# Kernel tuning notes

Hardware: AMD Instinct MI355X
Metric: run time of the kernel (lower is better)

Reference implementation:

```python
import jax, jax.numpy as jnp
import numpy as np

B, N, E = 2, 50000, 800000
IN, HID, OUT = 128, 64, 1
EPS = 1e-5


def setup_inputs() -> dict:
    key = jax.random.key(0)
    ks = jax.random.split(key, 13)
    x = jax.random.normal(ks[0], (B, N, IN), jnp.float32)
    edge_index = jax.random.randint(ks[1], (2, E), 0, N, dtype=jnp.int64)
    edge_weight = 0.1 * jax.random.normal(ks[2], (E,), jnp.float32)  # nn.Parameter, pre-exp
    W1 = jax.random.normal(ks[3], (IN, HID), jnp.float32) / np.sqrt(IN)
    b1 = jnp.zeros((HID,), jnp.float32)
    W2 = jax.random.normal(ks[4], (HID, HID), jnp.float32) / np.sqrt(HID)
    b2 = jnp.zeros((HID,), jnp.float32)
    g1 = jnp.ones((HID,), jnp.float32)
    be1 = jnp.zeros((HID,), jnp.float32)
    g2 = jnp.ones((HID,), jnp.float32)
    be2 = jnp.zeros((HID,), jnp.float32)
    Wc = jax.random.normal(ks[5], (HID, OUT), jnp.float32) / np.sqrt(HID)
    bc = jnp.zeros((OUT,), jnp.float32)
    return {"x": x, "edge_weight": edge_weight, "W1": W1, "b1": b1,
            "W2": W2, "b2": b2, "g1": g1, "be1": be1, "g2": g2, "be2": be2,
            "Wc": Wc, "bc": bc, "edge_index": edge_index}


def reference(x, edge_weight, W1, b1, W2, b2, g1, be1, g2, be2, Wc, bc, edge_index):
    n = x.shape[1]
    row, col = edge_index[0], edge_index[1]
    ew = jnp.exp(edge_weight)
    # GCN normalization with self-loops (fill_value=1), as in PyG gcn_norm
    loop = jnp.arange(n)
    rows = jnp.concatenate([row, loop])
    cols = jnp.concatenate([col, loop])
    w = jnp.concatenate([ew, jnp.ones((n,), ew.dtype)])
    deg = jax.ops.segment_sum(w, cols, num_segments=n)
    dinv = 1.0 / jnp.sqrt(deg)  # deg >= 1 due to self-loops
    norm = dinv[rows] * w * dinv[cols]  # [E+N]

    def conv(h, W, b):
        h = h @ W                                  # [B, N, H]
        msg = h[:, rows, :] * norm[None, :, None]  # gather + weight  [B, E+N, H]
        agg = jnp.zeros_like(h).at[:, cols, :].add(msg)  # scatter-add
        return agg + b

    def bn(h, g, be):  # BatchNorm1d over flattened (B*N, H), training-mode stats
        h2 = h.reshape(-1, h.shape[-1])
        m = h2.mean(axis=0)
        v = h2.var(axis=0)
        return (((h2 - m) / jnp.sqrt(v + EPS)) * g + be).reshape(h.shape)

    h = jax.nn.relu(conv(x, W1, b1))
    h = bn(h, g1, be1)  # dropout is identity in eval
    h = jax.nn.relu(conv(h, W2, b2))
    h = bn(h, g2, be2)
    out = (h @ Wc + bc)[..., 0]  # squeeze(-1) -> [B, N]
    return out
```

## Files before the change

kernel.cpp:

```cpp
#include <hip/hip_runtime.h>
#include <hip/hip_fp16.h>
#include <cstdint>
#include <cstddef>


#define CAP  64
#define OCAP 65536
#define BN_EPS 1e-5f

static __device__ __forceinline__ unsigned h2u(__half2 h) {
  union { __half2 h; unsigned u; } c; c.h = h; return c.u;
}
static __device__ __forceinline__ __half2 u2h(unsigned u) {
  union { unsigned u; __half2 h; } c; c.u = u; return c.h;
}
static __device__ __forceinline__ unsigned pack_pair(int src, float w) {
  __half hw = __float2half_rn(w);
  union { __half h; unsigned short s; } c; c.h = hw;
  return ((unsigned)src << 16) | c.s;
}
static __device__ __forceinline__ float pair_w(unsigned p) {
  union { unsigned short s; __half h; } c; c.s = (unsigned short)(p & 0xFFFFu);
  return __half2float(c.h);
}

__global__ void k_mega(const float* __restrict__ x, const float* __restrict__ W,
                       __half* __restrict__ out, int nrows, int N,
                       const float* __restrict__ ew, const int* __restrict__ ei,
                       int* __restrict__ cnt, unsigned* __restrict__ pairs,
                       int* __restrict__ ofl_cnt, int* __restrict__ ofl_list,
                       int E, int gemmBlocks, int fillBlocks) {
  constexpr int RT = 64, KC = 64, S = KC + 4;
  __shared__ float ws[KC * 64];
  __shared__ float xs[RT * S];

  int bid = blockIdx.x;
  int tid = threadIdx.x;
  int role = bid % 3;

  if (role == 0) {
    int gid = bid / 3;
    if (gid >= gemmBlocks) return;
    int row0 = gid * RT;
    int rg = tid >> 4, cg = tid & 15;
    int c0 = cg * 4, r0 = rg * 4;
    float acc[4][4];
#pragma unroll
    for (int i = 0; i < 4; ++i)
#pragma unroll
      for (int j = 0; j < 4; ++j) acc[i][j] = 0.0f;

    for (int ch = 0; ch < 2; ++ch) {
      if (ch) __syncthreads();
      const float4* Wp = (const float4*)(W + (size_t)ch * KC * 64);
      for (int s = tid; s < KC * 16; s += 256)
        ((float4*)ws)[s] = Wp[s];
      for (int s = tid; s < RT * 16; s += 256) {
        int r = s >> 4, k4 = s & 15;
        int gr = row0 + r;
        float4 v = make_float4(0.f, 0.f, 0.f, 0.f);
        if (gr < nrows)
          v = *(const float4*)(x + (size_t)gr * 128 + ch * KC + k4 * 4);
        *(float4*)&xs[r * S + k4 * 4] = v;
      }
      __syncthreads();
#pragma unroll 2
      for (int kk = 0; kk < KC; kk += 4) {
        float4 wv0 = *(const float4*)&ws[(kk + 0) * 64 + c0];
        float4 wv1 = *(const float4*)&ws[(kk + 1) * 64 + c0];
        float4 wv2 = *(const float4*)&ws[(kk + 2) * 64 + c0];
        float4 wv3 = *(const float4*)&ws[(kk + 3) * 64 + c0];
#pragma unroll
        for (int i = 0; i < 4; ++i) {
          float4 xv = *(const float4*)&xs[(r0 + i) * S + kk];
          acc[i][0] = fmaf(xv.x, wv0.x, acc[i][0]);
          acc[i][1] = fmaf(xv.x, wv0.y, acc[i][1]);
          acc[i][2] = fmaf(xv.x, wv0.z, acc[i][2]);
          acc[i][3] = fmaf(xv.x, wv0.w, acc[i][3]);
          acc[i][0] = fmaf(xv.y, wv1.x, acc[i][0]);
          acc[i][1] = fmaf(xv.y, wv1.y, acc[i][1]);
          acc[i][2] = fmaf(xv.y, wv1.z, acc[i][2]);
          acc[i][3] = fmaf(xv.y, wv1.w, acc[i][3]);
          acc[i][0] = fmaf(xv.z, wv2.x, acc[i][0]);
          acc[i][1] = fmaf(xv.z, wv2.y, acc[i][1]);
          acc[i][2] = fmaf(xv.z, wv2.z, acc[i][2]);
          acc[i][3] = fmaf(xv.z, wv2.w, acc[i][3]);
          acc[i][0] = fmaf(xv.w, wv3.x, acc[i][0]);
          acc[i][1] = fmaf(xv.w, wv3.y, acc[i][1]);
          acc[i][2] = fmaf(xv.w, wv3.z, acc[i][2]);
          acc[i][3] = fmaf(xv.w, wv3.w, acc[i][3]);
        }
      }
    }
#pragma unroll
    for (int i = 0; i < 4; ++i) {
      int gr = row0 + r0 + i;
      if (gr < nrows) {
        int orow = (gr < N) ? gr * 2 : (gr - N) * 2 + 1;
        __half2 h01 = __floats2half2_rn(acc[i][0], acc[i][1]);
        __half2 h23 = __floats2half2_rn(acc[i][2], acc[i][3]);
        *(uint2*)(out + (size_t)orow * 64 + c0) = make_uint2(h2u(h01), h2u(h23));
      }
    }
  } else {
    int fid = (bid / 3) * 2 + role - 1;
    if (fid >= fillBlocks) return;
    int e = fid * 256 + tid;
    if (e >= E) return;
    int r = ei[e];
    int c = ei[(size_t)E + e];
    float w = expf(ew[e]);
    int pos = atomicAdd(&cnt[c], 1);
    if (pos < CAP) {
      pairs[(size_t)c * CAP + pos] = pack_pair(r, w);
    } else {
      int o = atomicAdd(ofl_cnt, 1);
      if (o < OCAP) ofl_list[o] = e;
    }
  }
}

__global__ void k_degb(const unsigned* __restrict__ pairs, const int* __restrict__ cnt,
                       float* __restrict__ deg, int N) {
  int node = blockIdx.x * 4 + (threadIdx.x >> 6);
  if (node >= N) return;
  int lane = threadIdx.x & 63;
  int n = cnt[node];
  n = n > CAP ? CAP : n;
  float v = 0.0f;
  if (lane < n) v = pair_w(pairs[(size_t)node * CAP + lane]);
#pragma unroll
  for (int off = 32; off > 0; off >>= 1) v += __shfl_xor(v, off, 64);
  if (lane == 0) deg[node] = v + 1.0f;
}

__global__ void k_dego(const float* __restrict__ ew, const int* __restrict__ ei,
                       const int* __restrict__ ofl_cnt, const int* __restrict__ ofl_list,
                       float* __restrict__ deg, int E) {
  int tot = *ofl_cnt;
  if (tot > OCAP) tot = OCAP;
  for (int i = blockIdx.x * blockDim.x + threadIdx.x; i < tot;
       i += gridDim.x * blockDim.x) {
    int e = ofl_list[i];
    atomicAdd(&deg[ei[(size_t)E + e]], expf(ew[e]));
  }
}

__global__ void k_dinvf(float* __restrict__ deg, int N) {
  int i = blockIdx.x * blockDim.x + threadIdx.x;
  if (i < N) deg[i] = rsqrtf(deg[i]);
}

__global__ void k_gemm2(const __half* __restrict__ in, const float* __restrict__ W,
                        __half* __restrict__ out, int nrows,
                        const float* __restrict__ bias, const float* __restrict__ scsh) {
  constexpr int RT = 64, KC = 64, S = KC + 4;
  __shared__ float ws[KC * 64];
  __shared__ float xs[RT * S];

  int tid = threadIdx.x;
  int row0 = blockIdx.x * RT;
  for (int s = tid; s < KC * 16; s += 256)
    ((float4*)ws)[s] = ((const float4*)W)[s];
  for (int s = tid; s < RT * 16; s += 256) {
    int r = s >> 4, k4 = s & 15;
    int gr = row0 + r;
    int kg = k4 * 4;
    float4 v = make_float4(0.f, 0.f, 0.f, 0.f);
    if (gr < nrows) {
      uint2 u = *(const uint2*)(in + (size_t)gr * 64 + kg);
      float2 fa = __half22float2(u2h(u.x));
      float2 fb = __half22float2(u2h(u.y));
      v = make_float4(fa.x, fa.y, fb.x, fb.y);
    }
    float4 bb = *(const float4*)(bias + kg);
    float4 sc = *(const float4*)(scsh + kg);
    float4 sh = *(const float4*)(scsh + 64 + kg);
    v.x = fmaxf(v.x + bb.x, 0.f) * sc.x + sh.x;
    v.y = fmaxf(v.y + bb.y, 0.f) * sc.y + sh.y;
    v.z = fmaxf(v.z + bb.z, 0.f) * sc.z + sh.z;
    v.w = fmaxf(v.w + bb.w, 0.f) * sc.w + sh.w;
    *(float4*)&xs[r * S + kg] = v;
  }
  __syncthreads();

  int rg = tid >> 4, cg = tid & 15;
  int c0 = cg * 4, r0 = rg * 4;
  float acc[4][4];
#pragma unroll
  for (int i = 0; i < 4; ++i)
#pragma unroll
    for (int j = 0; j < 4; ++j) acc[i][j] = 0.0f;
#pragma unroll 2
  for (int kk = 0; kk < KC; kk += 4) {
    float4 wv0 = *(const float4*)&ws[(kk + 0) * 64 + c0];
    float4 wv1 = *(const float4*)&ws[(kk + 1) * 64 + c0];
    float4 wv2 = *(const float4*)&ws[(kk + 2) * 64 + c0];
    float4 wv3 = *(const float4*)&ws[(kk + 3) * 64 + c0];
#pragma unroll
    for (int i = 0; i < 4; ++i) {
      float4 xv = *(const float4*)&xs[(r0 + i) * S + kk];
      acc[i][0] = fmaf(xv.x, wv0.x, acc[i][0]);
      acc[i][1] = fmaf(xv.x, wv0.y, acc[i][1]);
      acc[i][2] = fmaf(xv.x, wv0.z, acc[i][2]);
      acc[i][3] = fmaf(xv.x, wv0.w, acc[i][3]);
      acc[i][0] = fmaf(xv.y, wv1.x, acc[i][0]);
      acc[i][1] = fmaf(xv.y, wv1.y, acc[i][1]);
      acc[i][2] = fmaf(xv.y, wv1.z, acc[i][2]);
      acc[i][3] = fmaf(xv.y, wv1.w, acc[i][3]);
      acc[i][0] = fmaf(xv.z, wv2.x, acc[i][0]);
      acc[i][1] = fmaf(xv.z, wv2.y, acc[i][1]);
      acc[i][2] = fmaf(xv.z, wv2.z, acc[i][2]);
      acc[i][3] = fmaf(xv.z, wv2.w, acc[i][3]);
      acc[i][0] = fmaf(xv.w, wv3.x, acc[i][0]);
      acc[i][1] = fmaf(xv.w, wv3.y, acc[i][1]);
      acc[i][2] = fmaf(xv.w, wv3.z, acc[i][2]);
      acc[i][3] = fmaf(xv.w, wv3.w, acc[i][3]);
    }
  }
#pragma unroll
  for (int i = 0; i < 4; ++i) {
    int gr = row0 + r0 + i;
    if (gr < nrows) {
      __half2 h01 = __floats2half2_rn(acc[i][0], acc[i][1]);
      __half2 h23 = __floats2half2_rn(acc[i][2], acc[i][3]);
      *(uint2*)(out + (size_t)gr * 64 + c0) = make_uint2(h2u(h01), h2u(h23));
    }
  }
}

__global__ void k_agg(const __half* __restrict__ h, const unsigned* __restrict__ pairs,
                      const int* __restrict__ cnt, const float* __restrict__ dinv,
                      __half* __restrict__ raw, int N) {
  int node = blockIdx.x * 4 + (threadIdx.x >> 6);
  if (node >= N) return;
  int lane = threadIdx.x & 63;
  const __half2* hv = (const __half2*)h;
  float dc = dinv[node];
  float2 self = __half22float2(hv[(size_t)node * 64 + lane]);
  float2 acc = make_float2(self.x * dc, self.y * dc);
  int n = cnt[node];
  n = n > CAP ? CAP : n;
  const unsigned* pp = pairs + (size_t)node * CAP;
  int k = 0;
  for (; k + 12 <= n; k += 12) {
    unsigned p[12];
#pragma unroll
    for (int q = 0; q < 12; ++q) p[q] = pp[k + q];
    float dr[12];
#pragma unroll
    for (int q = 0; q < 12; ++q) dr[q] = dinv[p[q] >> 16];
    __half2 v[12];
#pragma unroll
    for (int q = 0; q < 12; ++q) v[q] = hv[(size_t)(p[q] >> 16) * 64 + lane];
#pragma unroll
    for (int q = 0; q < 12; ++q) {
      float w = pair_w(p[q]) * dr[q];
      float2 f = __half22float2(v[q]);
      acc.x = fmaf(w, f.x, acc.x);
      acc.y = fmaf(w, f.y, acc.y);
    }
  }
  for (; k + 4 <= n; k += 4) {
    unsigned p[4];
#pragma unroll
    for (int q = 0; q < 4; ++q) p[q] = pp[k + q];
    float dr[4];
#pragma unroll
    for (int q = 0; q < 4; ++q) dr[q] = dinv[p[q] >> 16];
    __half2 v[4];
#pragma unroll
    for (int q = 0; q < 4; ++q) v[q] = hv[(size_t)(p[q] >> 16) * 64 + lane];
#pragma unroll
    for (int q = 0; q < 4; ++q) {
      float w = pair_w(p[q]) * dr[q];
      float2 f = __half22float2(v[q]);
      acc.x = fmaf(w, f.x, acc.x);
      acc.y = fmaf(w, f.y, acc.y);
    }
  }
  for (; k < n; ++k) {
    unsigned p = pp[k];
    float w = pair_w(p) * dinv[p >> 16];
    float2 f = __half22float2(hv[(size_t)(p >> 16) * 64 + lane]);
    acc.x = fmaf(w, f.x, acc.x);
    acc.y = fmaf(w, f.y, acc.y);
  }
  ((__half2*)raw)[(size_t)node * 64 + lane] =
      __floats2half2_rn(acc.x * dc, acc.y * dc);
}

__global__ void k_ofl(const float* __restrict__ ew, const int* __restrict__ ei,
                      const float* __restrict__ dinv, const int* __restrict__ ofl_cnt,
                      const int* __restrict__ ofl_list,
                      const __half* __restrict__ h, __half* __restrict__ raw,
                      int N, int E) {
  int tot = *ofl_cnt;
  if (tot > OCAP) tot = OCAP;
  for (int i = blockIdx.x * blockDim.x + threadIdx.x; i < tot;
       i += gridDim.x * blockDim.x) {
    int e = ofl_list[i];
    int r = ei[e];
    int c = ei[(size_t)E + e];
    float nrm = dinv[r] * expf(ew[e]) * dinv[c];
    const __half2* hr = (const __half2*)(h + (size_t)r * 128);
    unsigned* dst = (unsigned*)(raw + (size_t)c * 128);
    for (int j = 0; j < 64; ++j) {
      float2 hv2 = __half22float2(hr[j]);
      unsigned old = dst[j], assumed;
      do {
        assumed = old;
        float2 cur = __half22float2(u2h(assumed));
        __half2 nv = __floats2half2_rn(cur.x + nrm * hv2.x, cur.y + nrm * hv2.y);
        old = atomicCAS(&dst[j], assumed, h2u(nv));
      } while (old != assumed);
    }
  }
}

__global__ void k_stats(const __half* __restrict__ raw, const float* __restrict__ bias,
                        float* __restrict__ stats, const float* __restrict__ g,
                        const float* __restrict__ be, float* __restrict__ scsh,
                        int* __restrict__ done, float invCnt, int rows) {
  __shared__ float S[256], Q[256];
  __shared__ int isLast;
  int tid = threadIdx.x;
  int c = tid & 63, rg = tid >> 6;
  float s = 0.0f, q = 0.0f;
  for (int r = blockIdx.x * 4 + rg; r < rows; r += gridDim.x * 4) {
    float y = fmaxf(__half2float(raw[(size_t)r * 64 + c]) + bias[c], 0.0f);
    s += y;
    q += y * y;
  }
  S[tid] = s; Q[tid] = q;
  __syncthreads();
  if (tid < 64) {
    float ts = S[tid] + S[tid + 64] + S[tid + 128] + S[tid + 192];
    float tq = Q[tid] + Q[tid + 64] + Q[tid + 128] + Q[tid + 192];
    atomicAdd(&stats[tid], ts);
    atomicAdd(&stats[64 + tid], tq);
  }
  __threadfence();
  if (tid == 0) {
    int old = atomicAdd(done, 1);
    isLast = (old == (int)gridDim.x - 1);
  }
  __syncthreads();
  if (isLast && tid < 64) {
    __threadfence();
    float m = atomicAdd(&stats[tid], 0.0f) * invCnt;
    float qq = atomicAdd(&stats[64 + tid], 0.0f) * invCnt;
    float v = qq - m * m;
    v = v < 0.0f ? 0.0f : v;
    float inv = rsqrtf(v + BN_EPS);
    float sc = g[tid] * inv;
    scsh[tid] = sc;
    scsh[64 + tid] = be[tid] - m * sc;
  }
}

__global__ void k_out(const __half* __restrict__ raw, const float* __restrict__ bias,
                      const float* __restrict__ scsh, const float* __restrict__ Wc,
                      const float* __restrict__ bc, float* __restrict__ out,
                      int rows, int N) {
  int row = blockIdx.x * 4 + (threadIdx.x >> 6);
  int c = threadIdx.x & 63;
  if (row >= rows) return;
  float v = fmaxf(__half2float(raw[(size_t)row * 64 + c]) + bias[c], 0.0f)
              * scsh[c] + scsh[64 + c];
  float p = v * Wc[c];
#pragma unroll
  for (int off = 32; off > 0; off >>= 1) p += __shfl_xor(p, off, 64);
  if (c == 0) {
    int node = row >> 1, b = row & 1;
    out[(size_t)b * N + node] = p + bc[0];
  }
}

extern "C" void kernel_launch(void* const* d_in, const int* in_sizes, int n_in,
                              void* d_out, int out_size, void* d_ws, size_t ws_size,
                              hipStream_t stream) {
  const float* x   = (const float*)d_in[0];
  const float* ew  = (const float*)d_in[1];
  const float* W1  = (const float*)d_in[2];
  const float* b1  = (const float*)d_in[3];
  const float* W2  = (const float*)d_in[4];
  const float* b2  = (const float*)d_in[5];
  const float* g1  = (const float*)d_in[6];
  const float* be1 = (const float*)d_in[7];
  const float* g2  = (const float*)d_in[8];
  const float* be2 = (const float*)d_in[9];
  const float* Wc  = (const float*)d_in[10];
  const float* bc  = (const float*)d_in[11];
  const int*   ei  = (const int*)d_in[12];

  const int E  = in_sizes[1];
  const int BN = in_sizes[0] / 128;
  const int N  = BN / 2;

  char* w = (char*)d_ws;
  size_t off = 0;
  int*   cnt    = (int*)  (w + off); off += (size_t)N * 4;
  float* stats1 = (float*)(w + off); off += 512;
  float* stats2 = (float*)(w + off); off += 512;
  int*   oflc   = (int*)  (w + off); off += 16;
  int*   done1  = (int*)  (w + off); off += 16;
  int*   done2  = (int*)  (w + off); off += 16;
  size_t zbytes = off;
  float* dinv   = (float*)(w + off); off += (size_t)N * 4;
  float* scsh1  = (float*)(w + off); off += 512;
  float* scsh2  = (float*)(w + off); off += 512;
  int*   ofll   = (int*)  (w + off); off += (size_t)OCAP * 4;
  off = (off + 255) & ~(size_t)255;
  unsigned* pairs = (unsigned*)(w + off); off += (size_t)N * CAP * 4;
  __half* bufA  = (__half*)(w + off); off += (size_t)BN * 64 * 2;
  __half* bufB  = (__half*)(w + off); off += (size_t)BN * 64 * 2;

  float* out = (float*)d_out;

  hipMemsetAsync(w, 0, zbytes, stream);

  dim3 blk(256);
  int gB = (BN + 63) / 64;
  int fB = (E + 255) / 256;
  int base3 = gB > (fB + 1) / 2 ? gB : (fB + 1) / 2;
  int gMega = 3 * base3;
  int gN  = (N + 255) / 256;
  int gR  = (BN + 3) / 4;
  int gA  = (N + 3) / 4;

  k_mega<<<gMega, blk, 0, stream>>>(x, W1, bufA, BN, N, ew, ei, cnt, pairs,
                                    oflc, ofll, E, gB, fB);
  k_degb<<<gA, blk, 0, stream>>>(pairs, cnt, dinv, N);
  k_dego<<<16, blk, 0, stream>>>(ew, ei, oflc, ofll, dinv, E);
  k_dinvf<<<gN, blk, 0, stream>>>(dinv, N);

  k_agg<<<gA, blk, 0, stream>>>(bufA, pairs, cnt, dinv, bufB, N);
  k_ofl<<<16, blk, 0, stream>>>(ew, ei, dinv, oflc, ofll, bufA, bufB, N, E);
  k_stats<<<400, blk, 0, stream>>>(bufB, b1, stats1, g1, be1, scsh1, done1,
                                   1.0f / (float)BN, BN);

  k_gemm2<<<gB, blk, 0, stream>>>(bufB, W2, bufA, BN, b1, scsh1);
  k_agg<<<gA, blk, 0, stream>>>(bufA, pairs, cnt, dinv, bufB, N);
  k_ofl<<<16, blk, 0, stream>>>(ew, ei, dinv, oflc, ofll, bufA, bufB, N, E);
  k_stats<<<400, blk, 0, stream>>>(bufB, b2, stats2, g2, be2, scsh2, done2,
                                   1.0f / (float)BN, BN);

  k_out<<<gR, blk, 0, stream>>>(bufB, b2, scsh2, Wc, bc, out, BN, N);
}
```

Measured before the change: 366.5 us.

## Fuse whole GCN pipeline into one persistent cooperative kernel with grid syncs

Replaces the chain of about a dozen kernel launches with a single cooperative persistent kernel that walks through edge bucketing, GEMM1, degree computation, aggregation, BN statistics, GEMM2 and the output projection, separated by grid-wide syncs. BN statistics are now folded into the aggregation pass as per-block partial sums, removing the separate stats kernels and their global atomics. When overflow edges exist, a recompute pass runs after the fixup. This removes launch gaps and redundant reads of the aggregated buffer, but fixes the grid size to occupancy times 256 blocks (capped at 1024), so each phase gets lower parallelism and pays grid-sync overhead.

```diff
diff --git a/kernel.cpp b/kernel.cpp
--- a/kernel.cpp
+++ b/kernel.cpp
@@ -1,12 +1,16 @@
 #include <hip/hip_runtime.h>
 #include <hip/hip_fp16.h>
+#include <hip/hip_cooperative_groups.h>
 #include <cstdint>
 #include <cstddef>
+
+namespace cg = cooperative_groups;
 
 
 #define CAP  64
 #define OCAP 65536
 #define BN_EPS 1e-5f
+#define MAXB 1024
 
 static __device__ __forceinline__ unsigned h2u(__half2 h) {
   union { __half2 h; unsigned u; } c; c.h = h; return c.u;
@@ -24,182 +28,116 @@
   return __half2float(c.h);
 }
 
-__global__ void k_mega(const float* __restrict__ x, const float* __restrict__ W,
-                       __half* __restrict__ out, int nrows, int N,
-                       const float* __restrict__ ew, const int* __restrict__ ei,
-                       int* __restrict__ cnt, unsigned* __restrict__ pairs,
-                       int* __restrict__ ofl_cnt, int* __restrict__ ofl_list,
-                       int E, int gemmBlocks, int fillBlocks) {
-  constexpr int RT = 64, KC = 64, S = KC + 4;
-  __shared__ float ws[KC * 64];
-  __shared__ float xs[RT * S];
-
-  int bid = blockIdx.x;
-  int tid = threadIdx.x;
-  int role = bid % 3;
-
-  if (role == 0) {
-    int gid = bid / 3;
-    if (gid >= gemmBlocks) return;
-    int row0 = gid * RT;
-    int rg = tid >> 4, cg = tid & 15;
-    int c0 = cg * 4, r0 = rg * 4;
-    float acc[4][4];
-#pragma unroll
-    for (int i = 0; i < 4; ++i)
-#pragma unroll
-      for (int j = 0; j < 4; ++j) acc[i][j] = 0.0f;
-
-    for (int ch = 0; ch < 2; ++ch) {
-      if (ch) __syncthreads();
-      const float4* Wp = (const float4*)(W + (size_t)ch * KC * 64);
-      for (int s = tid; s < KC * 16; s += 256)
-        ((float4*)ws)[s] = Wp[s];
-      for (int s = tid; s < RT * 16; s += 256) {
-        int r = s >> 4, k4 = s & 15;
-        int gr = row0 + r;
-        float4 v = make_float4(0.f, 0.f, 0.f, 0.f);
-        if (gr < nrows)
-          v = *(const float4*)(x + (size_t)gr * 128 + ch * KC + k4 * 4);
-        *(float4*)&xs[r * S + k4 * 4] = v;
+struct Params {
+  const float* x; const float* ew;
+  const float* W1; const float* b1; const float* W2; const float* b2;
+  const float* g1; const float* be1; const float* g2; const float* be2;
+  const float* Wc; const float* bc; const int* ei;
+  int* cnt; int* oflc; int* ofll;
+  unsigned* pairs; float* dinv; float* pst;
+  float* scsh1; float* scsh2;
+  __half* bufA; __half* bufB; float* out;
+  int E, N, BN, gB;
+};
+
+static __device__ void gemm1_tile(const Params& p, int row0, float* ws, float* xs) {
+  const int tid = threadIdx.x;
+  __syncthreads();
+  int rg = tid >> 4, cgi = tid & 15, c0 = cgi * 4, r0 = rg * 4;
+  float acc[4][4];
+#pragma unroll
+  for (int i = 0; i < 4; ++i)
+#pragma unroll
+    for (int j = 0; j < 4; ++j) acc[i][j] = 0.0f;
+  for (int ch = 0; ch < 2; ++ch) {
+    if (ch) __syncthreads();
+    const float4* Wp = (const float4*)(p.W1 + (size_t)ch * 64 * 64);
+    for (int s = tid; s < 64 * 16; s += 256) ((float4*)ws)[s] = Wp[s];
+    for (int s = tid; s < 64 * 16; s += 256) {
+      int r = s >> 4, k4 = s & 15, gr = row0 + r;
+      float4 v = make_float4(0.f, 0.f, 0.f, 0.f);
+      if (gr < p.BN) v = *(const float4*)(p.x + (size_t)gr * 128 + ch * 64 + k4 * 4);
+      *(float4*)&xs[r * 68 + k4 * 4] = v;
+    }
+    __syncthreads();
+#pragma unroll 2
+    for (int kk = 0; kk < 64; kk += 4) {
+      float4 wv0 = *(const float4*)&ws[(kk + 0) * 64 + c0];
+      float4 wv1 = *(const float4*)&ws[(kk + 1) * 64 + c0];
+      float4 wv2 = *(const float4*)&ws[(kk + 2) * 64 + c0];
+      float4 wv3 = *(const float4*)&ws[(kk + 3) * 64 + c0];
+#pragma unroll
+      for (int i = 0; i < 4; ++i) {
+        float4 xv = *(const float4*)&xs[(r0 + i) * 68 + kk];
+        acc[i][0] = fmaf(xv.x, wv0.x, acc[i][0]);
+        acc[i][1] = fmaf(xv.x, wv0.y, acc[i][1]);
+        acc[i][2] = fmaf(xv.x, wv0.z, acc[i][2]);
+        acc[i][3] = fmaf(xv.x, wv0.w, acc[i][3]);
+        acc[i][0] = fmaf(xv.y, wv1.x, acc[i][0]);
+        acc[i][1] = fmaf(xv.y, wv1.y, acc[i][1]);
+        acc[i][2] = fmaf(xv.y, wv1.z, acc[i][2]);
+        acc[i][3] = fmaf(xv.y, wv1.w, acc[i][3]);
+        acc[i][0] = fmaf(xv.z, wv2.x, acc[i][0]);
+        acc[i][1] = fmaf(xv.z, wv2.y, acc[i][1]);
+        acc[i][2] = fmaf(xv.z, wv2.z, acc[i][2]);
+        acc[i][3] = fmaf(xv.z, wv2.w, acc[i][3]);
+        acc[i][0] = fmaf(xv.w, wv3.x, acc[i][0]);
+        acc[i][1] = fmaf(xv.w, wv3.y, acc[i][1]);
+        acc[i][2] = fmaf(xv.w, wv3.z, acc[i][2]);
+        acc[i][3] = fmaf(xv.w, wv3.w, acc[i][3]);
       }
-      __syncthreads();
-#pragma unroll 2
-      for (int kk = 0; kk < KC; kk += 4) {
-        float4 wv0 = *(const float4*)&ws[(kk + 0) * 64 + c0];
-        float4 wv1 = *(const float4*)&ws[(kk + 1) * 64 + c0];
-        float4 wv2 = *(const float4*)&ws[(kk + 2) * 64 + c0];
-        float4 wv3 = *(const float4*)&ws[(kk + 3) * 64 + c0];
-#pragma unroll
-        for (int i = 0; i < 4; ++i) {
-          float4 xv = *(const float4*)&xs[(r0 + i) * S + kk];
-          acc[i][0] = fmaf(xv.x, wv0.x, acc[i][0]);
-          acc[i][1] = fmaf(xv.x, wv0.y, acc[i][1]);
-          acc[i][2] = fmaf(xv.x, wv0.z, acc[i][2]);
-          acc[i][3] = fmaf(xv.x, wv0.w, acc[i][3]);
-          acc[i][0] = fmaf(xv.y, wv1.x, acc[i][0]);
-          acc[i][1] = fmaf(xv.y, wv1.y, acc[i][1]);
-          acc[i][2] = fmaf(xv.y, wv1.z, acc[i][2]);
-          acc[i][3] = fmaf(xv.y, wv1.w, acc[i][3]);
-          acc[i][0] = fmaf(xv.z, wv2.x, acc[i][0]);
-          acc[i][1] = fmaf(xv.z, wv2.y, acc[i][1]);
-          acc[i][2] = fmaf(xv.z, wv2.z, acc[i][2]);
-          acc[i][3] = fmaf(xv.z, wv2.w, acc[i][3]);
-          acc[i][0] = fmaf(xv.w, wv3.x, acc[i][0]);
-          acc[i][1] = fmaf(xv.w, wv3.y, acc[i][1]);
-          acc[i][2] = fmaf(xv.w, wv3.z, acc[i][2]);
-          acc[i][3] = fmaf(xv.w, wv3.w, acc[i][3]);
-        }
-      }
-    }
-#pragma unroll
-    for (int i = 0; i < 4; ++i) {
-      int gr = row0 + r0 + i;
-      if (gr < nrows) {
-        int orow = (gr < N) ? gr * 2 : (gr - N) * 2 + 1;
-        __half2 h01 = __floats2half2_rn(acc[i][0], acc[i][1]);
-        __half2 h23 = __floats2half2_rn(acc[i][2], acc[i][3]);
-        *(uint2*)(out + (size_t)orow * 64 + c0) = make_uint2(h2u(h01), h2u(h23));
-      }
-    }
-  } else {
-    int fid = (bid / 3) * 2 + role - 1;
-    if (fid >= fillBlocks) return;
-    int e = fid * 256 + tid;
-    if (e >= E) return;
-    int r = ei[e];
-    int c = ei[(size_t)E + e];
-    float w = expf(ew[e]);
-    int pos = atomicAdd(&cnt[c], 1);
-    if (pos < CAP) {
-      pairs[(size_t)c * CAP + pos] = pack_pair(r, w);
-    } else {
-      int o = atomicAdd(ofl_cnt, 1);
-      if (o < OCAP) ofl_list[o] = e;
-    }
-  }
-}
-
-__global__ void k_degb(const unsigned* __restrict__ pairs, const int* __restrict__ cnt,
-                       float* __restrict__ deg, int N) {
-  int node = blockIdx.x * 4 + (threadIdx.x >> 6);
-  if (node >= N) return;
-  int lane = threadIdx.x & 63;
-  int n = cnt[node];
-  n = n > CAP ? CAP : n;
-  float v = 0.0f;
-  if (lane < n) v = pair_w(pairs[(size_t)node * CAP + lane]);
-#pragma unroll
-  for (int off = 32; off > 0; off >>= 1) v += __shfl_xor(v, off, 64);
-  if (lane == 0) deg[node] = v + 1.0f;
-}
-
-__global__ void k_dego(const float* __restrict__ ew, const int* __restrict__ ei,
-                       const int* __restrict__ ofl_cnt, const int* __restrict__ ofl_list,
-                       float* __restrict__ deg, int E) {
-  int tot = *ofl_cnt;
-  if (tot > OCAP) tot = OCAP;
-  for (int i = blockIdx.x * blockDim.x + threadIdx.x; i < tot;
-       i += gridDim.x * blockDim.x) {
-    int e = ofl_list[i];
-    atomicAdd(&deg[ei[(size_t)E + e]], expf(ew[e]));
-  }
-}
-
-__global__ void k_dinvf(float* __restrict__ deg, int N) {
-  int i = blockIdx.x * blockDim.x + threadIdx.x;
-  if (i < N) deg[i] = rsqrtf(deg[i]);
-}
-
-__global__ void k_gemm2(const __half* __restrict__ in, const float* __restrict__ W,
-                        __half* __restrict__ out, int nrows,
-                        const float* __restrict__ bias, const float* __restrict__ scsh) {
-  constexpr int RT = 64, KC = 64, S = KC + 4;
-  __shared__ float ws[KC * 64];
-  __shared__ float xs[RT * S];
-
-  int tid = threadIdx.x;
-  int row0 = blockIdx.x * RT;
-  for (int s = tid; s < KC * 16; s += 256)
-    ((float4*)ws)[s] = ((const float4*)W)[s];
-  for (int s = tid; s < RT * 16; s += 256) {
-    int r = s >> 4, k4 = s & 15;
-    int gr = row0 + r;
-    int kg = k4 * 4;
+    }
+  }
+#pragma unroll
+  for (int i = 0; i < 4; ++i) {
+    int gr = row0 + r0 + i;
+    if (gr < p.BN) {
+      int orow = (gr < p.N) ? gr * 2 : (gr - p.N) * 2 + 1;
+      __half2 h01 = __floats2half2_rn(acc[i][0], acc[i][1]);
+      __half2 h23 = __floats2half2_rn(acc[i][2], acc[i][3]);
+      *(uint2*)(p.bufA + (size_t)orow * 64 + c0) = make_uint2(h2u(h01), h2u(h23));
+    }
+  }
+}
+
+static __device__ void gemm2_tile(const Params& p, int row0, float* ws, float* xs) {
+  const int tid = threadIdx.x;
+  __syncthreads();
+  for (int s = tid; s < 64 * 16; s += 256) ((float4*)ws)[s] = ((const float4*)p.W2)[s];
+  for (int s = tid; s < 64 * 16; s += 256) {
+    int r = s >> 4, k4 = s & 15, gr = row0 + r, kg = k4 * 4;
     float4 v = make_float4(0.f, 0.f, 0.f, 0.f);
-    if (gr < nrows) {
-      uint2 u = *(const uint2*)(in + (size_t)gr * 64 + kg);
+    if (gr < p.BN) {
+      uint2 u = *(const uint2*)(p.bufB + (size_t)gr * 64 + kg);
       float2 fa = __half22float2(u2h(u.x));
       float2 fb = __half22float2(u2h(u.y));
       v = make_float4(fa.x, fa.y, fb.x, fb.y);
     }
-    float4 bb = *(const float4*)(bias + kg);
-    float4 sc = *(const float4*)(scsh + kg);
-    float4 sh = *(const float4*)(scsh + 64 + kg);
+    float4 bb = *(const float4*)(p.b1 + kg);
+    float4 sc = *(const float4*)(p.scsh1 + kg);
+    float4 sh = *(const float4*)(p.scsh1 + 64 + kg);
     v.x = fmaxf(v.x + bb.x, 0.f) * sc.x + sh.x;
     v.y = fmaxf(v.y + bb.y, 0.f) * sc.y + sh.y;
     v.z = fmaxf(v.z + bb.z, 0.f) * sc.z + sh.z;
     v.w = fmaxf(v.w + bb.w, 0.f) * sc.w + sh.w;
-    *(float4*)&xs[r * S + kg] = v;
-  }
-  __syncthreads();
-
-  int rg = tid >> 4, cg = tid & 15;
-  int c0 = cg * 4, r0 = rg * 4;
+    *(float4*)&xs[r * 68 + kg] = v;
+  }
+  __syncthreads();
+  int rg = tid >> 4, cgi = tid & 15, c0 = cgi * 4, r0 = rg * 4;
   float acc[4][4];
 #pragma unroll
   for (int i = 0; i < 4; ++i)
 #pragma unroll
     for (int j = 0; j < 4; ++j) acc[i][j] = 0.0f;
 #pragma unroll 2
-  for (int kk = 0; kk < KC; kk += 4) {
+  for (int kk = 0; kk < 64; kk += 4) {
     float4 wv0 = *(const float4*)&ws[(kk + 0) * 64 + c0];
     float4 wv1 = *(const float4*)&ws[(kk + 1) * 64 + c0];
     float4 wv2 = *(const float4*)&ws[(kk + 2) * 64 + c0];
     float4 wv3 = *(const float4*)&ws[(kk + 3) * 64 + c0];
 #pragma unroll
     for (int i = 0; i < 4; ++i) {
-      float4 xv = *(const float4*)&xs[(r0 + i) * S + kk];
+      float4 xv = *(const float4*)&xs[(r0 + i) * 68 + kk];
       acc[i][0] = fmaf(xv.x, wv0.x, acc[i][0]);
       acc[i][1] = fmaf(xv.x, wv0.y, acc[i][1]);
       acc[i][2] = fmaf(xv.x, wv0.z, acc[i][2]);
@@ -221,88 +159,120 @@
 #pragma unroll
   for (int i = 0; i < 4; ++i) {
     int gr = row0 + r0 + i;
-    if (gr < nrows) {
+    if (gr < p.BN) {
       __half2 h01 = __floats2half2_rn(acc[i][0], acc[i][1]);
       __half2 h23 = __floats2half2_rn(acc[i][2], acc[i][3]);
-      *(uint2*)(out + (size_t)gr * 64 + c0) = make_uint2(h2u(h01), h2u(h23));
-    }
-  }
-}
-
-__global__ void k_agg(const __half* __restrict__ h, const unsigned* __restrict__ pairs,
-                      const int* __restrict__ cnt, const float* __restrict__ dinv,
-                      __half* __restrict__ raw, int N) {
-  int node = blockIdx.x * 4 + (threadIdx.x >> 6);
-  if (node >= N) return;
-  int lane = threadIdx.x & 63;
+      *(uint2*)(p.bufA + (size_t)gr * 64 + c0) = make_uint2(h2u(h01), h2u(h23));
+    }
+  }
+}
+
+static __device__ void agg_phase(const Params& p, const __half* h, __half* raw,
+                                 const float* bias, float* pst_out,
+                                 float* ws, float* xs, bool recompute) {
+  const int tid = threadIdx.x, lane = tid & 63;
+  const int nwav = gridDim.x * 4;
+  int gw = blockIdx.x * 4 + (tid >> 6);
   const __half2* hv = (const __half2*)h;
-  float dc = dinv[node];
-  float2 self = __half22float2(hv[(size_t)node * 64 + lane]);
-  float2 acc = make_float2(self.x * dc, self.y * dc);
-  int n = cnt[node];
-  n = n > CAP ? CAP : n;
-  const unsigned* pp = pairs + (size_t)node * CAP;
-  int k = 0;
-  for (; k + 12 <= n; k += 12) {
-    unsigned p[12];
-#pragma unroll
-    for (int q = 0; q < 12; ++q) p[q] = pp[k + q];
-    float dr[12];
-#pragma unroll
-    for (int q = 0; q < 12; ++q) dr[q] = dinv[p[q] >> 16];
-    __half2 v[12];
-#pragma unroll
-    for (int q = 0; q < 12; ++q) v[q] = hv[(size_t)(p[q] >> 16) * 64 + lane];
-#pragma unroll
-    for (int q = 0; q < 12; ++q) {
-      float w = pair_w(p[q]) * dr[q];
-      float2 f = __half22float2(v[q]);
-      acc.x = fmaf(w, f.x, acc.x);
-      acc.y = fmaf(w, f.y, acc.y);
-    }
-  }
-  for (; k + 4 <= n; k += 4) {
-    unsigned p[4];
-#pragma unroll
-    for (int q = 0; q < 4; ++q) p[q] = pp[k + q];
-    float dr[4];
-#pragma unroll
-    for (int q = 0; q < 4; ++q) dr[q] = dinv[p[q] >> 16];
-    __half2 v[4];
-#pragma unroll
-    for (int q = 0; q < 4; ++q) v[q] = hv[(size_t)(p[q] >> 16) * 64 + lane];
-#pragma unroll
-    for (int q = 0; q < 4; ++q) {
-      float w = pair_w(p[q]) * dr[q];
-      float2 f = __half22float2(v[q]);
-      acc.x = fmaf(w, f.x, acc.x);
-      acc.y = fmaf(w, f.y, acc.y);
-    }
-  }
-  for (; k < n; ++k) {
-    unsigned p = pp[k];
-    float w = pair_w(p) * dinv[p >> 16];
-    float2 f = __half22float2(hv[(size_t)(p >> 16) * 64 + lane]);
-    acc.x = fmaf(w, f.x, acc.x);
-    acc.y = fmaf(w, f.y, acc.y);
-  }
-  ((__half2*)raw)[(size_t)node * 64 + lane] =
-      __floats2half2_rn(acc.x * dc, acc.y * dc);
-}
-
-__global__ void k_ofl(const float* __restrict__ ew, const int* __restrict__ ei,
-                      const float* __restrict__ dinv, const int* __restrict__ ofl_cnt,
-                      const int* __restrict__ ofl_list,
-                      const __half* __restrict__ h, __half* __restrict__ raw,
-                      int N, int E) {
-  int tot = *ofl_cnt;
-  if (tot > OCAP) tot = OCAP;
-  for (int i = blockIdx.x * blockDim.x + threadIdx.x; i < tot;
-       i += gridDim.x * blockDim.x) {
-    int e = ofl_list[i];
-    int r = ei[e];
-    int c = ei[(size_t)E + e];
-    float nrm = dinv[r] * expf(ew[e]) * dinv[c];
+  __half2* rv = (__half2*)raw;
+  int cpp = 2 * (lane & 31);
+  float bb0 = bias[cpp], bb1 = bias[cpp + 1];
+  float sx = 0.f, sy = 0.f, qx = 0.f, qy = 0.f;
+  for (int node = gw; node < p.N; node += nwav) {
+    float vx, vy;
+    if (!recompute) {
+      float dc = p.dinv[node];
+      float2 self = __half22float2(hv[(size_t)node * 64 + lane]);
+      float ax = self.x * dc, ay = self.y * dc;
+      int n = p.cnt[node];
+      n = n > CAP ? CAP : n;
+      const unsigned* pp = p.pairs + (size_t)node * CAP;
+      int k = 0;
+      for (; k + 8 <= n; k += 8) {
+        unsigned pr[8];
+#pragma unroll
+        for (int q = 0; q < 8; ++q) pr[q] = pp[k + q];
+        float dr[8];
+#pragma unroll
+        for (int q = 0; q < 8; ++q) dr[q] = p.dinv[pr[q] >> 16];
+        __half2 vv[8];
+#pragma unroll
+        for (int q = 0; q < 8; ++q) vv[q] = hv[(size_t)(pr[q] >> 16) * 64 + lane];
+#pragma unroll
+        for (int q = 0; q < 8; ++q) {
+          float w = pair_w(pr[q]) * dr[q];
+          float2 f = __half22float2(vv[q]);
+          ax = fmaf(w, f.x, ax);
+          ay = fmaf(w, f.y, ay);
+        }
+      }
+      for (; k < n; ++k) {
+        unsigned pr = pp[k];
+        float w = pair_w(pr) * p.dinv[pr >> 16];
+        float2 f = __half22float2(hv[(size_t)(pr >> 16) * 64 + lane]);
+        ax = fmaf(w, f.x, ax);
+        ay = fmaf(w, f.y, ay);
+      }
+      vx = ax * dc; vy = ay * dc;
+      rv[(size_t)node * 64 + lane] = __floats2half2_rn(vx, vy);
+    } else {
+      float2 f = __half22float2(rv[(size_t)node * 64 + lane]);
+      vx = f.x; vy = f.y;
+    }
+    float y0 = fmaxf(vx + bb0, 0.f), y1 = fmaxf(vy + bb1, 0.f);
+    sx += y0; qx += y0 * y0;
+    sy += y1; qy += y1 * y1;
+  }
+  __syncthreads();
+  ws[tid] = sx; ws[256 + tid] = sy;
+  xs[tid] = qx; xs[256 + tid] = qy;
+  __syncthreads();
+  if (tid < 32) {
+    float a0 = 0, a1 = 0, b0 = 0, b1 = 0;
+    for (int j = tid; j < 256; j += 32) {
+      a0 += ws[j]; a1 += ws[256 + j];
+      b0 += xs[j]; b1 += xs[256 + j];
+    }
+    pst_out[2 * tid] = a0;      pst_out[2 * tid + 1] = a1;
+    pst_out[64 + 2 * tid] = b0; pst_out[64 + 2 * tid + 1] = b1;
+  }
+  __syncthreads();
+}
+
+static __device__ void scsh_phase(const Params& p, const float* g, const float* be,
+                                  float* scsh, float* ws, float invCnt) {
+  const int tid = threadIdx.x, bid = blockIdx.x;
+  if (bid < 64) {
+    float s = 0.f, q = 0.f;
+    for (int b = tid; b < (int)gridDim.x; b += 256) {
+      s += p.pst[(size_t)b * 128 + bid];
+      q += p.pst[(size_t)b * 128 + 64 + bid];
+    }
+    __syncthreads();
+    ws[tid] = s; ws[256 + tid] = q;
+    __syncthreads();
+    for (int o = 128; o; o >>= 1) {
+      if (tid < o) { ws[tid] += ws[tid + o]; ws[256 + tid] += ws[256 + tid + o]; }
+      __syncthreads();
+    }
+    if (tid == 0) {
+      float m = ws[0] * invCnt;
+      float v = ws[256] * invCnt - m * m;
+      v = v < 0.f ? 0.f : v;
+      float inv = rsqrtf(v + BN_EPS);
+      float sc = g[bid] * inv;
+      scsh[bid] = sc;
+      scsh[64 + bid] = be[bid] - m * sc;
+    }
+  }
+}
+
+static __device__ void ofl_fix(const Params& p, const __half* h, __half* raw, int tot) {
+  int gtid = blockIdx.x * 256 + threadIdx.x, gsz = gridDim.x * 256;
+  for (int i = gtid; i < tot; i += gsz) {
+    int e = p.ofll[i];
+    int r = p.ei[e], c = p.ei[(size_t)p.E + e];
+    float nrm = p.dinv[r] * expf(p.ew[e]) * p.dinv[c];
     const __half2* hr = (const __half2*)(h + (size_t)r * 128);
     unsigned* dst = (unsigned*)(raw + (size_t)c * 128);
     for (int j = 0; j < 64; ++j) {
@@ -318,133 +288,142 @@
   }
 }
 
-__global__ void k_stats(const __half* __restrict__ raw, const float* __restrict__ bias,
-                        float* __restrict__ stats, const float* __restrict__ g,
-                        const float* __restrict__ be, float* __restrict__ scsh,
-                        int* __restrict__ done, float invCnt, int rows) {
-  __shared__ float S[256], Q[256];
-  __shared__ int isLast;
-  int tid = threadIdx.x;
-  int c = tid & 63, rg = tid >> 6;
-  float s = 0.0f, q = 0.0f;
-  for (int r = blockIdx.x * 4 + rg; r < rows; r += gridDim.x * 4) {
-    float y = fmaxf(__half2float(raw[(size_t)r * 64 + c]) + bias[c], 0.0f);
-    s += y;
-    q += y * y;
-  }
-  S[tid] = s; Q[tid] = q;
-  __syncthreads();
-  if (tid < 64) {
-    float ts = S[tid] + S[tid + 64] + S[tid + 128] + S[tid + 192];
-    float tq = Q[tid] + Q[tid + 64] + Q[tid + 128] + Q[tid + 192];
-    atomicAdd(&stats[tid], ts);
-    atomicAdd(&stats[64 + tid], tq);
-  }
-  __threadfence();
-  if (tid == 0) {
-    int old = atomicAdd(done, 1);
-    isLast = (old == (int)gridDim.x - 1);
-  }
-  __syncthreads();
-  if (isLast && tid < 64) {
-    __threadfence();
-    float m = atomicAdd(&stats[tid], 0.0f) * invCnt;
-    float qq = atomicAdd(&stats[64 + tid], 0.0f) * invCnt;
-    float v = qq - m * m;
-    v = v < 0.0f ? 0.0f : v;
-    float inv = rsqrtf(v + BN_EPS);
-    float sc = g[tid] * inv;
-    scsh[tid] = sc;
-    scsh[64 + tid] = be[tid] - m * sc;
-  }
-}
-
-__global__ void k_out(const __half* __restrict__ raw, const float* __restrict__ bias,
-                      const float* __restrict__ scsh, const float* __restrict__ Wc,
-                      const float* __restrict__ bc, float* __restrict__ out,
-                      int rows, int N) {
-  int row = blockIdx.x * 4 + (threadIdx.x >> 6);
-  int c = threadIdx.x & 63;
-  if (row >= rows) return;
-  float v = fmaxf(__half2float(raw[(size_t)row * 64 + c]) + bias[c], 0.0f)
-              * scsh[c] + scsh[64 + c];
-  float p = v * Wc[c];
-#pragma unroll
-  for (int off = 32; off > 0; off >>= 1) p += __shfl_xor(p, off, 64);
-  if (c == 0) {
-    int node = row >> 1, b = row & 1;
-    out[(size_t)b * N + node] = p + bc[0];
+__global__ __launch_bounds__(256, 4)
+void k_coop(Params p) {
+  cg::grid_group grid = cg::this_grid();
+  __shared__ float ws[64 * 64];
+  __shared__ float xs[64 * 68];
+  const int tid = threadIdx.x;
+  const int nb = gridDim.x;
+  const int gsz = nb * 256;
+  const int gtid = blockIdx.x * 256 + tid;
+  float* myPst = p.pst + (size_t)blockIdx.x * 128;
+
+  for (int e = gtid; e < p.E; e += gsz) {
+    int r = p.ei[e], c = p.ei[(size_t)p.E + e];
+    float w = expf(p.ew[e]);
+    int pos = atomicAdd(&p.cnt[c], 1);
+    if (pos < CAP) p.pairs[(size_t)c * CAP + pos] = pack_pair(r, w);
+    else { int o = atomicAdd(p.oflc, 1); if (o < OCAP) p.ofll[o] = e; }
+  }
+  for (int t = blockIdx.x; t < p.gB; t += nb) gemm1_tile(p, t * 64, ws, xs);
+  grid.sync();
+
+  int tot = *p.oflc;
+  if (tot > OCAP) tot = OCAP;
+  {
+    int gw = blockIdx.x * 4 + (tid >> 6), lane = tid & 63, nwav = nb * 4;
+    for (int node = gw; node < p.N; node += nwav) {
+      int n = p.cnt[node];
+      n = n > CAP ? CAP : n;
+      float v = 0.f;
+      if (lane < n) v = pair_w(p.pairs[(size_t)node * CAP + lane]);
+#pragma unroll
+      for (int o = 32; o; o >>= 1) v += __shfl_xor(v, o, 64);
+      if (lane == 0) p.dinv[node] = (tot == 0) ? rsqrtf(v + 1.0f) : (v + 1.0f);
+    }
+  }
+  if (tot > 0) {
+    grid.sync();
+    for (int i = gtid; i < tot; i += gsz) {
+      int e = p.ofll[i];
+      atomicAdd(&p.dinv[p.ei[(size_t)p.E + e]], expf(p.ew[e]));
+    }
+    grid.sync();
+    for (int i = gtid; i < p.N; i += gsz) p.dinv[i] = rsqrtf(p.dinv[i]);
+  }
+  grid.sync();
+
+  agg_phase(p, p.bufA, p.bufB, p.b1, myPst, ws, xs, false);
+  if (tot > 0) {
+    grid.sync();
+    ofl_fix(p, p.bufA, p.bufB, tot);
+    grid.sync();
+    agg_phase(p, p.bufA, p.bufB, p.b1, myPst, ws, xs, true);
+  }
+  grid.sync();
+  scsh_phase(p, p.g1, p.be1, p.scsh1, ws, 1.0f / (float)p.BN);
+  grid.sync();
+
+  for (int t = blockIdx.x; t < p.gB; t += nb) gemm2_tile(p, t * 64, ws, xs);
+  grid.sync();
+
+  agg_phase(p, p.bufA, p.bufB, p.b2, myPst, ws, xs, false);
+  if (tot > 0) {
+    grid.sync();
+    ofl_fix(p, p.bufA, p.bufB, tot);
+    grid.sync();
+    agg_phase(p, p.bufA, p.bufB, p.b2, myPst, ws, xs, true);
+  }
+  grid.sync();
+  scsh_phase(p, p.g2, p.be2, p.scsh2, ws, 1.0f / (float)p.BN);
+  grid.sync();
+
+  {
+    int gw = blockIdx.x * 4 + (tid >> 6), c = tid & 63, nwav = nb * 4;
+    for (int row = gw; row < p.BN; row += nwav) {
+      float v = fmaxf(__half2float(p.bufB[(size_t)row * 64 + c]) + p.b2[c], 0.f)
+                  * p.scsh2[c] + p.scsh2[64 + c];
+      float q = v * p.Wc[c];
+#pragma unroll
+      for (int o = 32; o; o >>= 1) q += __shfl_xor(q, o, 64);
+      if (c == 0) {
+        int node = row >> 1, b = row & 1;
+        p.out[(size_t)b * p.N + node] = q + p.bc[0];
+      }
+    }
   }
 }
 
 extern "C" void kernel_launch(void* const* d_in, const int* in_sizes, int n_in,
                               void* d_out, int out_size, void* d_ws, size_t ws_size,
                               hipStream_t stream) {
-  const float* x   = (const float*)d_in[0];
-  const float* ew  = (const float*)d_in[1];
-  const float* W1  = (const float*)d_in[2];
-  const float* b1  = (const float*)d_in[3];
-  const float* W2  = (const float*)d_in[4];
-  const float* b2  = (const float*)d_in[5];
-  const float* g1  = (const float*)d_in[6];
-  const float* be1 = (const float*)d_in[7];
-  const float* g2  = (const float*)d_in[8];
-  const float* be2 = (const float*)d_in[9];
-  const float* Wc  = (const float*)d_in[10];
-  const float* bc  = (const float*)d_in[11];
-  const int*   ei  = (const int*)d_in[12];
+  Params prm;
+  prm.x   = (const float*)d_in[0];
+  prm.ew  = (const float*)d_in[1];
+  prm.W1  = (const float*)d_in[2];
+  prm.b1  = (const float*)d_in[3];
+  prm.W2  = (const float*)d_in[4];
+  prm.b2  = (const float*)d_in[5];
+  prm.g1  = (const float*)d_in[6];
+  prm.be1 = (const float*)d_in[7];
+  prm.g2  = (const float*)d_in[8];
+  prm.be2 = (const float*)d_in[9];
+  prm.Wc  = (const float*)d_in[10];
+  prm.bc  = (const float*)d_in[11];
+  prm.ei  = (const int*)d_in[12];
 
   const int E  = in_sizes[1];
   const int BN = in_sizes[0] / 128;
   const int N  = BN / 2;
+  prm.E = E; prm.N = N; prm.BN = BN;
+  prm.gB = (BN + 63) / 64;
 
   char* w = (char*)d_ws;
   size_t off = 0;
-  int*   cnt    = (int*)  (w + off); off += (size_t)N * 4;
-  float* stats1 = (float*)(w + off); off += 512;
-  float* stats2 = (float*)(w + off); off += 512;
-  int*   oflc   = (int*)  (w + off); off += 16;
-  int*   done1  = (int*)  (w + off); off += 16;
-  int*   done2  = (int*)  (w + off); off += 16;
+  prm.cnt  = (int*)(w + off);   off += (size_t)N * 4;
+  prm.oflc = (int*)(w + off);   off += 16;
   size_t zbytes = off;
-  float* dinv   = (float*)(w + off); off += (size_t)N * 4;
-  float* scsh1  = (float*)(w + off); off += 512;
-  float* scsh2  = (float*)(w + off); off += 512;
-  int*   ofll   = (int*)  (w + off); off += (size_t)OCAP * 4;
+  prm.dinv  = (float*)(w + off); off += (size_t)N * 4;
+  prm.scsh1 = (float*)(w + off); off += 512;
+  prm.scsh2 = (float*)(w + off); off += 512;
+  prm.ofll  = (int*)(w + off);   off += (size_t)OCAP * 4;
   off = (off + 255) & ~(size_t)255;
-  unsigned* pairs = (unsigned*)(w + off); off += (size_t)N * CAP * 4;
-  __half* bufA  = (__half*)(w + off); off += (size_t)BN * 64 * 2;
-  __half* bufB  = (__half*)(w + off); off += (size_t)BN * 64 * 2;
-
-  float* out = (float*)d_out;
+  prm.pst   = (float*)(w + off); off += (size_t)MAXB * 128 * 4;
+  prm.pairs = (unsigned*)(w + off); off += (size_t)N * CAP * 4;
+  prm.bufA  = (__half*)(w + off);   off += (size_t)BN * 64 * 2;
+  prm.bufB  = (__half*)(w + off);   off += (size_t)BN * 64 * 2;
+  prm.out   = (float*)d_out;
 
   hipMemsetAsync(w, 0, zbytes, stream);
 
-  dim3 blk(256);
-  int gB = (BN + 63) / 64;
-  int fB = (E + 255) / 256;
-  int base3 = gB > (fB + 1) / 2 ? gB : (fB + 1) / 2;
-  int gMega = 3 * base3;
-  int gN  = (N + 255) / 256;
-  int gR  = (BN + 3) / 4;
-  int gA  = (N + 3) / 4;
-
-  k_mega<<<gMega, blk, 0, stream>>>(x, W1, bufA, BN, N, ew, ei, cnt, pairs,
-                                    oflc, ofll, E, gB, fB);
-  k_degb<<<gA, blk, 0, stream>>>(pairs, cnt, dinv, N);
-  k_dego<<<16, blk, 0, stream>>>(ew, ei, oflc, ofll, dinv, E);
-  k_dinvf<<<gN, blk, 0, stream>>>(dinv, N);
-
-  k_agg<<<gA, blk, 0, stream>>>(bufA, pairs, cnt, dinv, bufB, N);
-  k_ofl<<<16, blk, 0, stream>>>(ew, ei, dinv, oflc, ofll, bufA, bufB, N, E);
-  k_stats<<<400, blk, 0, stream>>>(bufB, b1, stats1, g1, be1, scsh1, done1,
-                                   1.0f / (float)BN, BN);
-
-  k_gemm2<<<gB, blk, 0, stream>>>(bufB, W2, bufA, BN, b1, scsh1);
-  k_agg<<<gA, blk, 0, stream>>>(bufA, pairs, cnt, dinv, bufB, N);
-  k_ofl<<<16, blk, 0, stream>>>(ew, ei, dinv, oflc, ofll, bufA, bufB, N, E);
-  k_stats<<<400, blk, 0, stream>>>(bufB, b2, stats2, g2, be2, scsh2, done2,
-                                   1.0f / (float)BN, BN);
-
-  k_out<<<gR, blk, 0, stream>>>(bufB, b2, scsh2, Wc, bc, out, BN, N);
-}
+  int occ = 0;
+  hipOccupancyMaxActiveBlocksPerMultiprocessor(&occ, (const void*)k_coop, 256, 0);
+  if (occ < 1) occ = 1;
+  int grid = occ * 256;
+  if (grid > MAXB) grid = MAXB;
+
+  void* kargs[] = { (void*)&prm };
+  hipLaunchCooperativeKernel((const void*)k_coop, dim3(grid), dim3(256),
+                             kargs, 0, stream);
+}
```

After: 876.8 us. +139.3%, slower.
